# Performance work log

Measured on AMD Instinct MI355X. Metric: run time of the kernel, lower is better.

The kernel has to match this reference:

```python
import jax, jax.numpy as jnp
import numpy as np

N_NODES = 20000
N_EDGES = 320000
N_GRAPHS = 64
NEG_SLOPE = 0.2
BN_EPS = 1e-5


def setup_inputs() -> dict:
    key = jax.random.key(0)
    ks = jax.random.split(key, 32)
    inp = {}
    inp['x'] = jax.random.normal(ks[0], (N_NODES, 9), jnp.float32)
    inp['global_feat'] = jax.random.normal(ks[1], (N_GRAPHS, 20), jnp.float32)
    inp['edge_index'] = jax.random.randint(ks[2], (2, N_EDGES), 0, N_NODES, jnp.int32)
    inp['batch'] = jnp.sort(jax.random.randint(ks[3], (N_NODES,), 0, N_GRAPHS, jnp.int32))
    s = 0.1  # modest init scale for numerical sanity
    inp['W_l1'] = jax.random.normal(ks[4], (9, 256), jnp.float32) * s
    inp['b_l1'] = jax.random.normal(ks[5], (256,), jnp.float32) * s
    inp['W_r1'] = jax.random.normal(ks[6], (9, 256), jnp.float32) * s
    inp['b_r1'] = jax.random.normal(ks[7], (256,), jnp.float32) * s
    inp['att1'] = jax.random.normal(ks[8], (4, 64), jnp.float32) * s
    inp['bias1'] = jax.random.normal(ks[9], (256,), jnp.float32) * s
    inp['bn1_gamma'] = jnp.ones((256,), jnp.float32)
    inp['bn1_beta'] = jnp.zeros((256,), jnp.float32)
    inp['bn1_mean'] = jax.random.normal(ks[10], (256,), jnp.float32) * s
    inp['bn1_var'] = jax.random.uniform(ks[11], (256,), jnp.float32, 0.5, 1.5)
    inp['W_l2'] = jax.random.normal(ks[12], (256, 512), jnp.float32) * s
    inp['b_l2'] = jax.random.normal(ks[13], (512,), jnp.float32) * s
    inp['W_r2'] = jax.random.normal(ks[14], (256, 512), jnp.float32) * s
    inp['b_r2'] = jax.random.normal(ks[15], (512,), jnp.float32) * s
    inp['att2'] = jax.random.normal(ks[16], (4, 128), jnp.float32) * s
    inp['bias2'] = jax.random.normal(ks[17], (512,), jnp.float32) * s
    inp['bn2_gamma'] = jnp.ones((512,), jnp.float32)
    inp['bn2_beta'] = jnp.zeros((512,), jnp.float32)
    inp['bn2_mean'] = jax.random.normal(ks[18], (512,), jnp.float32) * s
    inp['bn2_var'] = jax.random.uniform(ks[19], (512,), jnp.float32, 0.5, 1.5)
    inp['fc1_W'] = jax.random.normal(ks[20], (532, 128), jnp.float32) * s
    inp['fc1_b'] = jax.random.normal(ks[21], (128,), jnp.float32) * s
    inp['fc2_W'] = jax.random.normal(ks[22], (128, 1), jnp.float32) * s
    inp['fc2_b'] = jax.random.normal(ks[23], (1,), jnp.float32) * s
    return inp


def _gatv2(x, src, dst, W_l, b_l, W_r, b_r, att, bias, H, C):
    N = x.shape[0]
    xl = (x @ W_l + b_l).reshape(N, H, C)  # source transform
    xr = (x @ W_r + b_r).reshape(N, H, C)  # target transform
    m = xl[src] + xr[dst]                               # [E,H,C]
    e = jnp.sum(jax.nn.leaky_relu(m, NEG_SLOPE) * att, axis=-1)  # [E,H]
    emax = jax.ops.segment_max(e, dst, num_segments=N)
    ex = jnp.exp(e - emax[dst])
    denom = jax.ops.segment_sum(ex, dst, num_segments=N)
    alpha = ex / denom[dst]                             # segment softmax over incoming edges
    out = jax.ops.segment_sum(alpha[..., None] * xl[src], dst, num_segments=N)
    return out.reshape(N, H * C) + bias


def _bn_eval(x, gamma, beta, mean, var):
    return (x - mean) * jax.lax.rsqrt(var + BN_EPS) * gamma + beta


def reference(x, global_feat, edge_index, batch,
              W_l1, b_l1, W_r1, b_r1, att1, bias1,
              bn1_gamma, bn1_beta, bn1_mean, bn1_var,
              W_l2, b_l2, W_r2, b_r2, att2, bias2,
              bn2_gamma, bn2_beta, bn2_mean, bn2_var,
              fc1_W, fc1_b, fc2_W, fc2_b):
    N = x.shape[0]
    # PyG GATv2Conv default: add self loops
    loop = jnp.arange(N, dtype=edge_index.dtype)
    src = jnp.concatenate([edge_index[0], loop])
    dst = jnp.concatenate([edge_index[1], loop])
    h = _gatv2(x, src, dst, W_l1, b_l1, W_r1, b_r1, att1, bias1, 4, 64)
    h = jax.nn.relu(_bn_eval(h, bn1_gamma, bn1_beta, bn1_mean, bn1_var))
    h = _gatv2(h, src, dst, W_l2, b_l2, W_r2, b_r2, att2, bias2, 4, 128)
    h = jax.nn.relu(_bn_eval(h, bn2_gamma, bn2_beta, bn2_mean, bn2_var))
    # global mean pool over graphs
    B = global_feat.shape[0]
    sums = jax.ops.segment_sum(h, batch, num_segments=B)
    cnts = jax.ops.segment_sum(jnp.ones((N, 1), h.dtype), batch, num_segments=B)
    pooled = sums / jnp.maximum(cnts, 1.0)
    z = jnp.concatenate([pooled, global_feat], axis=1)  # [B, 532]
    z = jax.nn.relu(z @ fc1_W + fc1_b)  # dropout is identity at inference
    return (z @ fc2_W + fc2_b).squeeze(-1)  # [B]
```

## Files before the change

### kernel.cpp

```cpp
#include <hip/hip_runtime.h>


typedef _Float16 half2v __attribute__((ext_vector_type(2)));
typedef _Float16 half8v __attribute__((ext_vector_type(8)));
typedef __attribute__((ext_vector_type(4))) float floatx4;

#define SLOT_STRIDE 96

template <int CPL> struct VecSel;
template <> struct VecSel<4> { using T = uint2; };
template <> struct VecSel<8> { using T = uint4; };

__device__ inline unsigned short f2h(float v) {
    return __builtin_bit_cast(unsigned short, (_Float16)v);
}
__device__ inline half2v u2h2(unsigned u) { return __builtin_bit_cast(half2v, u); }
__device__ inline unsigned h22u(half2v h) { return __builtin_bit_cast(unsigned, h); }
__device__ inline unsigned packh2(float a, float b) {
    half2v h; h[0] = (_Float16)a; h[1] = (_Float16)b;
    return h22u(h);
}

__device__ inline float fdot2f(half2v a, half2v b, float c) {
#if __has_builtin(__builtin_amdgcn_fdot2)
    return __builtin_amdgcn_fdot2(a, b, c, false);
#else
    return c + (float)a[0] * (float)b[0] + (float)a[1] * (float)b[1];
#endif
}


#define L1_NODES 32

__global__ void k_setup(const int* __restrict__ ei, int E0, int N, int B,
                        int* __restrict__ counts, int* __restrict__ slots,
                        const int* __restrict__ batch, int* __restrict__ goff,
                        const float* __restrict__ x,
                        const float* __restrict__ Wl1, const float* __restrict__ bl1,
                        const float* __restrict__ Wr1, const float* __restrict__ br1,
                        unsigned short* __restrict__ xl1, unsigned short* __restrict__ xr1,
                        const float* __restrict__ Wl2, const float* __restrict__ Wr2,
                        unsigned short* __restrict__ Wlt, unsigned short* __restrict__ Wrt) {
    __shared__ char smem[8320];
    int E = E0 + N;
    int SC = (E + 255) >> 8;
    int L1B = (N + L1_NODES - 1) / L1_NODES;
    int bid = blockIdx.x;
    int t = threadIdx.x;

    if (bid < SC) {
        int e = bid * 256 + t;
        if (e >= E) return;
        int s, d;
        if (e < E0) { s = ei[e]; d = ei[E0 + e]; } else { s = e - E0; d = s; }
        int pos = atomicAdd(&counts[d], 1);
        if (pos < SLOT_STRIDE) slots[d * SLOT_STRIDE + pos] = s;
    } else if (bid < SC + L1B) {
        float (*xs)[9] = reinterpret_cast<float(*)[9]>(smem);
        int nb = (bid - SC) * L1_NODES;
        int h = t >> 7, p = t & 127;
        for (int i = t; i < L1_NODES * 9; i += 256) {
            int node = nb + i / 9;
            xs[i / 9][i % 9] = (node < N) ? x[node * 9 + i % 9] : 0.f;
        }
        __syncthreads();
        int c0 = 2 * p, c1 = 2 * p + 1;
        float wl0[9], wl1[9], wr0[9], wr1[9];
#pragma unroll
        for (int k = 0; k < 9; k++) {
            wl0[k] = Wl1[k * 256 + c0]; wl1[k] = Wl1[k * 256 + c1];
            wr0[k] = Wr1[k * 256 + c0]; wr1[k] = Wr1[k * 256 + c1];
        }
        float b0 = bl1[c0], b1 = bl1[c1], r0b = br1[c0], r1b = br1[c1];
        for (int j = h * 16; j < h * 16 + 16; j++) {
            int node = nb + j;
            if (node >= N) break;
            float a0 = b0, a1 = b1, r0 = r0b, r1 = r1b;
#pragma unroll
            for (int k = 0; k < 9; k++) {
                float xv = xs[j][k];
                a0 += xv * wl0[k]; a1 += xv * wl1[k];
                r0 += xv * wr0[k]; r1 += xv * wr1[k];
            }
            *reinterpret_cast<unsigned*>(xl1 + (size_t)node * 256 + c0) = packh2(a0, a1);
            *reinterpret_cast<unsigned*>(xr1 + (size_t)node * 256 + c0) = packh2(r0, r1);
        }
    } else if (bid < SC + L1B + 64) {
        unsigned short (*tile)[65] = reinterpret_cast<unsigned short(*)[65]>(smem);
        int idx = bid - SC - L1B;
        int tx = idx & 7, ty = (idx >> 3) & 3, tz = idx >> 5;
        const float* W = tz ? Wr2 : Wl2;
        unsigned short* Wt = tz ? Wrt : Wlt;
        int k0 = ty * 64, n0 = tx * 64;
        int tn = t & 63, tq = t >> 6;
#pragma unroll
        for (int i = 0; i < 16; i++) {
            int k = tq * 16 + i;
            tile[k][tn] = f2h(W[(size_t)(k0 + k) * 512 + n0 + tn]);
        }
        __syncthreads();
#pragma unroll
        for (int i = 0; i < 16; i++) {
            int nn = tq * 16 + i;
            Wt[(size_t)(n0 + nn) * 256 + k0 + tn] = tile[tn][nn];
        }
    } else {
        int n = (bid - SC - L1B - 64) * 256 + t;
        if (n >= N) return;
        int b = batch[n];
        int prev = (n == 0) ? -1 : batch[n - 1];
        for (int g = prev + 1; g <= b; g++) goff[g] = n;
        if (n == N - 1)
            for (int g = b + 1; g <= B; g++) goff[g] = N;
    }
}


template <int CPL>
__global__ void k_gat_agg(const unsigned short* __restrict__ xl,
                          const unsigned short* __restrict__ xr,
                          const float* __restrict__ att, const float* __restrict__ bias,
                          const float* __restrict__ gamma, const float* __restrict__ beta,
                          const float* __restrict__ mean, const float* __restrict__ var,
                          const int* __restrict__ counts, const int* __restrict__ slots,
                          unsigned short* __restrict__ hout, int N) {
    const int HC = 64 * CPL;
    const int V = CPL / 2;
    using VecT = typename VecSel<CPL>::T;
    int wave = (blockIdx.x * blockDim.x + threadIdx.x) >> 6;
    int lane = threadIdx.x & 63;
    if (wave >= N) return;
    int n = wave;
    int cbase = lane * CPL;

    half2v xr2[V], at2[V], acc[V];
    {
        unsigned r[V];
        if constexpr (CPL == 8) {
            uint4 q = *reinterpret_cast<const uint4*>(xr + (size_t)n * HC + cbase);
            r[0] = q.x; r[1] = q.y; r[2] = q.z; r[3] = q.w;
        } else {
            uint2 q = *reinterpret_cast<const uint2*>(xr + (size_t)n * HC + cbase);
            r[0] = q.x; r[1] = q.y;
        }
#pragma unroll
        for (int v = 0; v < V; v++) {
            xr2[v] = u2h2(r[v]);
            at2[v][0] = (_Float16)att[cbase + 2 * v];
            at2[v][1] = (_Float16)att[cbase + 2 * v + 1];
            acc[v] = (half2v){(_Float16)0.f, (_Float16)0.f};
        }
    }
    const half2v c02 = {(_Float16)0.2f, (_Float16)0.2f};

    int deg = counts[n];
    deg = deg < SLOT_STRIDE ? deg : SLOT_STRIDE;
    const int* sl = slots + (size_t)n * SLOT_STRIDE;
    const unsigned short* xlb = xl + cbase;
    float m = -1e30f, l = 0.f;

    VecT qA = *reinterpret_cast<const VecT*>(xlb + (size_t)sl[0] * HC);
    VecT qB = (deg > 1) ? *reinterpret_cast<const VecT*>(xlb + (size_t)sl[1] * HC) : qA;

    int slot = 0;
    while (slot + 1 < deg) {
        VecT ra = qA, rb = qB;
        int p2 = slot + 2 < deg ? slot + 2 : deg - 1;
        int p3 = slot + 3 < deg ? slot + 3 : deg - 1;
        qA = *reinterpret_cast<const VecT*>(xlb + (size_t)sl[p2] * HC);
        qB = *reinterpret_cast<const VecT*>(xlb + (size_t)sl[p3] * HC);

        half2v ah[V], bh[V];
        {
            unsigned ua[V], ub[V];
            if constexpr (CPL == 8) {
                ua[0] = ra.x; ua[1] = ra.y; ua[2] = ra.z; ua[3] = ra.w;
                ub[0] = rb.x; ub[1] = rb.y; ub[2] = rb.z; ub[3] = rb.w;
            } else {
                ua[0] = ra.x; ua[1] = ra.y;
                ub[0] = rb.x; ub[1] = rb.y;
            }
#pragma unroll
            for (int v = 0; v < V; v++) { ah[v] = u2h2(ua[v]); bh[v] = u2h2(ub[v]); }
        }
        float pa = 0.f, pb = 0.f;
#pragma unroll
        for (int v = 0; v < V; v++) {
            half2v ta = ah[v] + xr2[v];
            half2v la = __builtin_elementwise_max(ta, ta * c02);
            pa = fdot2f(la, at2[v], pa);
            half2v tb = bh[v] + xr2[v];
            half2v lb = __builtin_elementwise_max(tb, tb * c02);
            pb = fdot2f(lb, at2[v], pb);
        }
        pa += __shfl_xor(pa, 1);  pb += __shfl_xor(pb, 1);
        pa += __shfl_xor(pa, 2);  pb += __shfl_xor(pb, 2);
        pa += __shfl_xor(pa, 4);  pb += __shfl_xor(pb, 4);
        pa += __shfl_xor(pa, 8);  pb += __shfl_xor(pb, 8);
        float pm = fmaxf(pa, pb);
        if (__all(pm <= m + 4.f)) {
            float wa = __expf(pa - m), wb = __expf(pb - m);
            l += wa + wb;
            _Float16 wah = (_Float16)wa, wbh = (_Float16)wb;
            half2v wa2 = {wah, wah}, wb2 = {wbh, wbh};
#pragma unroll
            for (int v = 0; v < V; v++) {
                acc[v] = ah[v] * wa2 + acc[v];
                acc[v] = bh[v] * wb2 + acc[v];
            }
        } else {
            float mn = fmaxf(m, pm);
            float sc = __expf(m - mn);
            float wa = __expf(pa - mn), wb = __expf(pb - mn);
            l = l * sc + wa + wb;
            _Float16 sch = (_Float16)sc, wah = (_Float16)wa, wbh = (_Float16)wb;
            half2v sc2 = {sch, sch}, wa2 = {wah, wah}, wb2 = {wbh, wbh};
#pragma unroll
            for (int v = 0; v < V; v++) {
                acc[v] = ah[v] * wa2 + acc[v] * sc2;
                acc[v] = bh[v] * wb2 + acc[v];
            }
            m = mn;
        }
        slot += 2;
    }
    if (slot < deg) {
        half2v ah[V];
        {
            unsigned ua[V];
            if constexpr (CPL == 8) {
                ua[0] = qA.x; ua[1] = qA.y; ua[2] = qA.z; ua[3] = qA.w;
            } else {
                ua[0] = qA.x; ua[1] = qA.y;
            }
#pragma unroll
            for (int v = 0; v < V; v++) ah[v] = u2h2(ua[v]);
        }
        float pa = 0.f;
#pragma unroll
        for (int v = 0; v < V; v++) {
            half2v ta = ah[v] + xr2[v];
            half2v la = __builtin_elementwise_max(ta, ta * c02);
            pa = fdot2f(la, at2[v], pa);
        }
        pa += __shfl_xor(pa, 1);
        pa += __shfl_xor(pa, 2);
        pa += __shfl_xor(pa, 4);
        pa += __shfl_xor(pa, 8);
        if (__all(pa <= m + 4.f)) {
            float wa = __expf(pa - m);
            l += wa;
            _Float16 wah = (_Float16)wa;
            half2v wa2 = {wah, wah};
#pragma unroll
            for (int v = 0; v < V; v++) acc[v] = ah[v] * wa2 + acc[v];
        } else {
            float mn = fmaxf(m, pa);
            float sc = __expf(m - mn);
            float wa = __expf(pa - mn);
            l = l * sc + wa;
            _Float16 sch = (_Float16)sc, wah = (_Float16)wa;
            half2v sc2 = {sch, sch}, wa2 = {wah, wah};
#pragma unroll
            for (int v = 0; v < V; v++) acc[v] = ah[v] * wa2 + acc[v] * sc2;
            m = mn;
        }
    }

    float inv = 1.f / l;
    unsigned ow[V];
#pragma unroll
    for (int v = 0; v < V; v++) {
        half2v o;
#pragma unroll
        for (int j = 0; j < 2; j++) {
            int c = cbase + 2 * v + j;
            float val = (float)acc[v][j] * inv + bias[c];
            val = (val - mean[c]) * rsqrtf(var[c] + 1e-5f) * gamma[c] + beta[c];
            o[j] = (_Float16)fmaxf(val, 0.f);
        }
        ow[v] = h22u(o);
    }
    unsigned short* dst = hout + (size_t)n * HC + cbase;
    if constexpr (CPL == 8)
        *reinterpret_cast<uint4*>(dst) = *reinterpret_cast<uint4*>(ow);
    else
        *reinterpret_cast<uint2*>(dst) = *reinterpret_cast<uint2*>(ow);
}


__global__ __launch_bounds__(256) void k_gemm_mfma(
    const unsigned short* __restrict__ A,
    const unsigned short* __restrict__ Wlt,
    const unsigned short* __restrict__ Wrt,
    const float* __restrict__ bl, const float* __restrict__ br,
    unsigned short* __restrict__ Cl, unsigned short* __restrict__ Cr,
    int M) {
    const int K = 256, NCOL = 512;
    __shared__ unsigned short lds[2][2][128 * 32];
    int side = blockIdx.z;
    const unsigned short* Bmat = side ? Wrt : Wlt;
    const float* bias = side ? br : bl;
    unsigned short* C = side ? Cr : Cl;
    int bm = blockIdx.y * 128, bn = blockIdx.x * 128;
    int t = threadIdx.x;
    int lane = t & 63;
    int wid = t >> 6;
    int wr = wid >> 1, wc = wid & 1;

    floatx4 acc[4][4];
#pragma unroll
    for (int m = 0; m < 4; m++)
#pragma unroll
        for (int n = 0; n < 4; n++) acc[m][n] = (floatx4){0.f, 0.f, 0.f, 0.f};

    auto stage = [&](int buf, int k0) {
#pragma unroll
        for (int i = 0; i < 2; i++) {
            int c = i * 256 + t;
            int row = c >> 2;
            int kk = ((c & 3) << 3) ^ (((row >> 1) & 3) << 3);
            int gm = bm + row; gm = gm < M ? gm : M - 1;
            const unsigned short* gA = A + (size_t)gm * K + k0 + kk;
            __builtin_amdgcn_global_load_lds(
                (const __attribute__((address_space(1))) void*)gA,
                (__attribute__((address_space(3))) void*)&lds[buf][0][c * 8], 16, 0, 0);
            int gn = bn + row;
            const unsigned short* gB = Bmat + (size_t)gn * K + k0 + kk;
            __builtin_amdgcn_global_load_lds(
                (const __attribute__((address_space(1))) void*)gB,
                (__attribute__((address_space(3))) void*)&lds[buf][1][c * 8], 16, 0, 0);
        }
    };

    stage(0, 0);
    __syncthreads();
    int q = lane >> 4, rl = lane & 15;
    for (int ks = 0; ks < 8; ks++) {
        int buf = ks & 1;
        if (ks < 7) stage(buf ^ 1, (ks + 1) * 32);
        half8v a[4], b[4];
#pragma unroll
        for (int m = 0; m < 4; m++) {
            int row = wr * 64 + m * 16 + rl;
            int colb = (q * 16) ^ (((row >> 1) & 3) << 4);
            a[m] = *reinterpret_cast<const half8v*>(
                reinterpret_cast<const char*>(&lds[buf][0][0]) + row * 64 + colb);
        }
#pragma unroll
        for (int n = 0; n < 4; n++) {
            int row = wc * 64 + n * 16 + rl;
            int colb = (q * 16) ^ (((row >> 1) & 3) << 4);
            b[n] = *reinterpret_cast<const half8v*>(
                reinterpret_cast<const char*>(&lds[buf][1][0]) + row * 64 + colb);
        }
#pragma unroll
        for (int m = 0; m < 4; m++)
#pragma unroll
            for (int n = 0; n < 4; n++)
                acc[m][n] = __builtin_amdgcn_mfma_f32_16x16x32_f16(a[m], b[n], acc[m][n], 0, 0, 0);
        __syncthreads();
    }
#pragma unroll
    for (int m = 0; m < 4; m++) {
#pragma unroll
        for (int n = 0; n < 4; n++) {
            int gn = bn + wc * 64 + n * 16 + rl;
            float bv = bias[gn];
#pragma unroll
            for (int r = 0; r < 4; r++) {
                int gm = bm + wr * 64 + m * 16 + q * 4 + r;
                if (gm < M) C[(size_t)gm * NCOL + gn] = f2h(acc[m][n][r] + bv);
            }
        }
    }
}


#define POOL_CHUNKS 32

__global__ void k_pool_partial(const unsigned short* __restrict__ h2,
                               const int* __restrict__ goff,
                               float* __restrict__ partial) {
    int g = blockIdx.x, c = blockIdx.y;
    int t = threadIdx.x;
    int n0 = goff[g], n1 = goff[g + 1];
    int len = n1 - n0;
    int c0 = n0 + (int)(((long long)len * c) / POOL_CHUNKS);
    int c1 = n0 + (int)(((long long)len * (c + 1)) / POOL_CHUNKS);
    float s0 = 0.f, s1 = 0.f;
    for (int n = c0; n < c1; n++) {
        half2v h = u2h2(*reinterpret_cast<const unsigned*>(h2 + (size_t)n * 512 + t * 2));
        s0 += (float)h[0]; s1 += (float)h[1];
    }
    float* p = partial + ((size_t)g * POOL_CHUNKS + c) * 512;
    p[t * 2] = s0;
    p[t * 2 + 1] = s1;
}


__global__ void k_pool_head(const float* __restrict__ partial,
                            const int* __restrict__ goff,
                            const float* __restrict__ gf,
                            const float* __restrict__ W1, const float* __restrict__ b1,
                            const float* __restrict__ W2, const float* __restrict__ b2,
                            float* __restrict__ out) {
    int g = blockIdx.x;
    int t = threadIdx.x;
    __shared__ float z[532];
    __shared__ float red[128];
    float s = 0.f;
#pragma unroll
    for (int c = 0; c < POOL_CHUNKS; c++)
        s += partial[((size_t)g * POOL_CHUNKS + c) * 512 + t];
    float inv = 1.f / fmaxf((float)(goff[g + 1] - goff[g]), 1.f);
    z[t] = s * inv;
    if (t < 20) z[512 + t] = gf[g * 20 + t];
    __syncthreads();
    if (t < 128) {
        float a = b1[t];
        for (int k = 0; k < 532; k++) a += z[k] * W1[k * 128 + t];
        red[t] = fmaxf(a, 0.f) * W2[t];
    }
    __syncthreads();
    if (t < 64) {
        float v = red[t] + red[t + 64];
#pragma unroll
        for (int sdown = 32; sdown; sdown >>= 1) v += __shfl_down(v, sdown);
        if (t == 0) out[g] = v + b2[0];
    }
}


extern "C" void kernel_launch(void* const* d_in, const int* in_sizes, int n_in,
                              void* d_out, int out_size, void* d_ws, size_t ws_size,
                              hipStream_t stream) {
    const float* x       = (const float*)d_in[0];
    const float* gfeat   = (const float*)d_in[1];
    const int*   ei      = (const int*)d_in[2];
    const int*   batch   = (const int*)d_in[3];
    const float* W_l1    = (const float*)d_in[4];
    const float* b_l1    = (const float*)d_in[5];
    const float* W_r1    = (const float*)d_in[6];
    const float* b_r1    = (const float*)d_in[7];
    const float* att1    = (const float*)d_in[8];
    const float* bias1   = (const float*)d_in[9];
    const float* bn1_g   = (const float*)d_in[10];
    const float* bn1_b   = (const float*)d_in[11];
    const float* bn1_m   = (const float*)d_in[12];
    const float* bn1_v   = (const float*)d_in[13];
    const float* W_l2    = (const float*)d_in[14];
    const float* b_l2    = (const float*)d_in[15];
    const float* W_r2    = (const float*)d_in[16];
    const float* b_r2    = (const float*)d_in[17];
    const float* att2    = (const float*)d_in[18];
    const float* bias2   = (const float*)d_in[19];
    const float* bn2_g   = (const float*)d_in[20];
    const float* bn2_b   = (const float*)d_in[21];
    const float* bn2_m   = (const float*)d_in[22];
    const float* bn2_v   = (const float*)d_in[23];
    const float* fc1_W   = (const float*)d_in[24];
    const float* fc1_b   = (const float*)d_in[25];
    const float* fc2_W   = (const float*)d_in[26];
    const float* fc2_b   = (const float*)d_in[27];
    float* out = (float*)d_out;

    const int N  = in_sizes[0] / 9;
    const int B  = in_sizes[1] / 20;
    const int E0 = in_sizes[2] / 2;
    const int E  = E0 + N;

    char* ws = (char*)d_ws;
    const size_t SZ256 = (size_t)N * 256 * 2;
    const size_t SZ512 = (size_t)N * 512 * 2;
    unsigned short* xl1 = (unsigned short*)(ws);
    unsigned short* xr1 = (unsigned short*)(ws + SZ256);
    unsigned short* h1  = (unsigned short*)(ws + 2 * SZ256);
    unsigned short* xl2 = (unsigned short*)(ws + 3 * SZ256);
    unsigned short* xr2 = (unsigned short*)(ws + 3 * SZ256 + SZ512);
    unsigned short* h2  = (unsigned short*)(ws + 3 * SZ256 + 2 * SZ512);
    size_t o = 3 * SZ256 + 3 * SZ512;
    unsigned short* Wlt = (unsigned short*)(ws + o);
    unsigned short* Wrt = (unsigned short*)(ws + o + 262144);
    size_t oi = o + 2 * 262144;
    int* counts = (int*)(ws + oi);
    int* goff   = (int*)(ws + oi + 80000);
    int* slots  = (int*)(ws + oi + 80000 + 384);
    size_t op = oi + 80000 + 384 + (size_t)N * SLOT_STRIDE * 4;
    float* partial = (float*)(ws + op);
    (void)ws_size; (void)n_in; (void)out_size;

    (void)hipMemsetAsync(ws + oi, 0, 80000, stream);

    int SC = (E + 255) / 256;
    int L1B = (N + L1_NODES - 1) / L1_NODES;
    int GB = (N + 255) / 256;
    k_setup<<<SC + L1B + 64 + GB, 256, 0, stream>>>(
        ei, E0, N, B, counts, slots, batch, goff,
        x, W_l1, b_l1, W_r1, b_r1, xl1, xr1, W_l2, W_r2, Wlt, Wrt);

    k_gat_agg<4><<<(N * 64 + 255) / 256, 256, 0, stream>>>(
        xl1, xr1, att1, bias1, bn1_g, bn1_b, bn1_m, bn1_v, counts, slots, h1, N);

    dim3 ggrid(512 / 128, (N + 127) / 128, 2);
    k_gemm_mfma<<<ggrid, 256, 0, stream>>>(h1, Wlt, Wrt, b_l2, b_r2, xl2, xr2, N);

    k_gat_agg<8><<<(N * 64 + 255) / 256, 256, 0, stream>>>(
        xl2, xr2, att2, bias2, bn2_g, bn2_b, bn2_m, bn2_v, counts, slots, h2, N);

    k_pool_partial<<<dim3(B, POOL_CHUNKS), 256, 0, stream>>>(h2, goff, partial);
    k_pool_head<<<B, 512, 0, stream>>>(partial, goff, gfeat,
                                       fc1_W, fc1_b, fc2_W, fc2_b, out);
}
```

Baseline: 170.2 us.

## Sort nodes by degree and use persistent grid-stride waves in GAT aggregation

Adds a single-block counting-sort kernel that orders nodes by in-degree. Both aggregation kernels become persistent, with a fixed grid of 2048 blocks whose waves loop over nodes in that degree order. The aim is to balance work, since waves in a block then handle similar degrees and tail imbalance shrinks. The cost is an extra serial single-block launch, plus less locality for the xr reads and hout writes.

Result: slower. 193.6 us (+13.7%).

```diff
diff --git a/kernel.cpp b/kernel.cpp
--- a/kernel.cpp
+++ b/kernel.cpp
@@ -6,6 +6,7 @@
 typedef __attribute__((ext_vector_type(4))) float floatx4;
 
 #define SLOT_STRIDE 96
+#define AGG_BLOCKS 2048
 
 template <int CPL> struct VecSel;
 template <> struct VecSel<4> { using T = uint2; };
@@ -116,176 +117,206 @@
 }
 
 
+__global__ void k_degsort(const int* __restrict__ counts, int* __restrict__ order, int N) {
+    __shared__ int bins[128];
+    __shared__ int base[128];
+    int t = threadIdx.x;
+    if (t < 128) bins[t] = 0;
+    __syncthreads();
+    for (int n = t; n < N; n += 1024) {
+        int d = counts[n]; d = d > 96 ? 96 : d;
+        atomicAdd(&bins[d], 1);
+    }
+    __syncthreads();
+    if (t == 0) {
+        int s = 0;
+        for (int i = 0; i < 128; i++) { base[i] = s; s += bins[i]; }
+    }
+    __syncthreads();
+    if (t < 128) bins[t] = 0;
+    __syncthreads();
+    for (int n = t; n < N; n += 1024) {
+        int d = counts[n]; d = d > 96 ? 96 : d;
+        int p = atomicAdd(&bins[d], 1);
+        order[base[d] + p] = n;
+    }
+}
+
+
 template <int CPL>
-__global__ void k_gat_agg(const unsigned short* __restrict__ xl,
-                          const unsigned short* __restrict__ xr,
-                          const float* __restrict__ att, const float* __restrict__ bias,
-                          const float* __restrict__ gamma, const float* __restrict__ beta,
-                          const float* __restrict__ mean, const float* __restrict__ var,
-                          const int* __restrict__ counts, const int* __restrict__ slots,
-                          unsigned short* __restrict__ hout, int N) {
+__global__ __launch_bounds__(256) void k_gat_agg(
+        const unsigned short* __restrict__ xl,
+        const unsigned short* __restrict__ xr,
+        const float* __restrict__ att, const float* __restrict__ bias,
+        const float* __restrict__ gamma, const float* __restrict__ beta,
+        const float* __restrict__ mean, const float* __restrict__ var,
+        const int* __restrict__ counts, const int* __restrict__ slots,
+        const int* __restrict__ order,
+        unsigned short* __restrict__ hout, int N) {
     const int HC = 64 * CPL;
     const int V = CPL / 2;
     using VecT = typename VecSel<CPL>::T;
-    int wave = (blockIdx.x * blockDim.x + threadIdx.x) >> 6;
+    int gw = (blockIdx.x * blockDim.x + threadIdx.x) >> 6;
     int lane = threadIdx.x & 63;
-    if (wave >= N) return;
-    int n = wave;
+    const int GW = AGG_BLOCKS * 4;
     int cbase = lane * CPL;
 
-    half2v xr2[V], at2[V], acc[V];
-    {
-        unsigned r[V];
-        if constexpr (CPL == 8) {
-            uint4 q = *reinterpret_cast<const uint4*>(xr + (size_t)n * HC + cbase);
-            r[0] = q.x; r[1] = q.y; r[2] = q.z; r[3] = q.w;
-        } else {
-            uint2 q = *reinterpret_cast<const uint2*>(xr + (size_t)n * HC + cbase);
-            r[0] = q.x; r[1] = q.y;
-        }
+    half2v at2[V];
+#pragma unroll
+    for (int v = 0; v < V; v++) {
+        at2[v][0] = (_Float16)att[cbase + 2 * v];
+        at2[v][1] = (_Float16)att[cbase + 2 * v + 1];
+    }
+    const half2v c02 = {(_Float16)0.2f, (_Float16)0.2f};
+
+    for (int i = gw; i < N; i += GW) {
+        int n = order[i];
+        half2v xr2[V], acc[V];
+        {
+            VecT q = *reinterpret_cast<const VecT*>(xr + (size_t)n * HC + cbase);
+            unsigned r[V];
+            if constexpr (CPL == 8) { r[0] = q.x; r[1] = q.y; r[2] = q.z; r[3] = q.w; }
+            else { r[0] = q.x; r[1] = q.y; }
+#pragma unroll
+            for (int v = 0; v < V; v++) {
+                xr2[v] = u2h2(r[v]);
+                acc[v] = (half2v){(_Float16)0.f, (_Float16)0.f};
+            }
+        }
+        int deg = counts[n];
+        deg = deg < SLOT_STRIDE ? deg : SLOT_STRIDE;
+        const int* sl = slots + (size_t)n * SLOT_STRIDE;
+        const unsigned short* xlb = xl + cbase;
+        float m = -1e30f, l = 0.f;
+
+        VecT qA = *reinterpret_cast<const VecT*>(xlb + (size_t)sl[0] * HC);
+        VecT qB = (deg > 1) ? *reinterpret_cast<const VecT*>(xlb + (size_t)sl[1] * HC) : qA;
+
+        int slot = 0;
+        while (slot + 1 < deg) {
+            VecT ra = qA, rb = qB;
+            int p2 = slot + 2 < deg ? slot + 2 : deg - 1;
+            int p3 = slot + 3 < deg ? slot + 3 : deg - 1;
+            qA = *reinterpret_cast<const VecT*>(xlb + (size_t)sl[p2] * HC);
+            qB = *reinterpret_cast<const VecT*>(xlb + (size_t)sl[p3] * HC);
+
+            half2v ah[V], bh[V];
+            {
+                unsigned ua[V], ub[V];
+                if constexpr (CPL == 8) {
+                    ua[0] = ra.x; ua[1] = ra.y; ua[2] = ra.z; ua[3] = ra.w;
+                    ub[0] = rb.x; ub[1] = rb.y; ub[2] = rb.z; ub[3] = rb.w;
+                } else {
+                    ua[0] = ra.x; ua[1] = ra.y;
+                    ub[0] = rb.x; ub[1] = rb.y;
+                }
+#pragma unroll
+                for (int v = 0; v < V; v++) { ah[v] = u2h2(ua[v]); bh[v] = u2h2(ub[v]); }
+            }
+            float pa = 0.f, pb = 0.f;
+#pragma unroll
+            for (int v = 0; v < V; v++) {
+                half2v ta = ah[v] + xr2[v];
+                half2v la = __builtin_elementwise_max(ta, ta * c02);
+                pa = fdot2f(la, at2[v], pa);
+                half2v tb = bh[v] + xr2[v];
+                half2v lb = __builtin_elementwise_max(tb, tb * c02);
+                pb = fdot2f(lb, at2[v], pb);
+            }
+            pa += __shfl_xor(pa, 1);  pb += __shfl_xor(pb, 1);
+            pa += __shfl_xor(pa, 2);  pb += __shfl_xor(pb, 2);
+            pa += __shfl_xor(pa, 4);  pb += __shfl_xor(pb, 4);
+            pa += __shfl_xor(pa, 8);  pb += __shfl_xor(pb, 8);
+            float pm = fmaxf(pa, pb);
+            if (__all(pm <= m + 4.f)) {
+                float wa = __expf(pa - m), wb = __expf(pb - m);
+                l += wa + wb;
+                _Float16 wah = (_Float16)wa, wbh = (_Float16)wb;
+                half2v wa2 = {wah, wah}, wb2 = {wbh, wbh};
+#pragma unroll
+                for (int v = 0; v < V; v++) {
+                    acc[v] = ah[v] * wa2 + acc[v];
+                    acc[v] = bh[v] * wb2 + acc[v];
+                }
+            } else {
+                float mn = fmaxf(m, pm);
+                float sc = __expf(m - mn);
+                float wa = __expf(pa - mn), wb = __expf(pb - mn);
+                l = l * sc + wa + wb;
+                _Float16 sch = (_Float16)sc, wah = (_Float16)wa, wbh = (_Float16)wb;
+                half2v sc2 = {sch, sch}, wa2 = {wah, wah}, wb2 = {wbh, wbh};
+#pragma unroll
+                for (int v = 0; v < V; v++) {
+                    acc[v] = ah[v] * wa2 + acc[v] * sc2;
+                    acc[v] = bh[v] * wb2 + acc[v];
+                }
+                m = mn;
+            }
+            slot += 2;
+        }
+        if (slot < deg) {
+            half2v ah[V];
+            {
+                unsigned ua[V];
+                if constexpr (CPL == 8) {
+                    ua[0] = qA.x; ua[1] = qA.y; ua[2] = qA.z; ua[3] = qA.w;
+                } else {
+                    ua[0] = qA.x; ua[1] = qA.y;
+                }
+#pragma unroll
+                for (int v = 0; v < V; v++) ah[v] = u2h2(ua[v]);
+            }
+            float pa = 0.f;
+#pragma unroll
+            for (int v = 0; v < V; v++) {
+                half2v ta = ah[v] + xr2[v];
+                half2v la = __builtin_elementwise_max(ta, ta * c02);
+                pa = fdot2f(la, at2[v], pa);
+            }
+            pa += __shfl_xor(pa, 1);
+            pa += __shfl_xor(pa, 2);
+            pa += __shfl_xor(pa, 4);
+            pa += __shfl_xor(pa, 8);
+            if (__all(pa <= m + 4.f)) {
+                float wa = __expf(pa - m);
+                l += wa;
+                _Float16 wah = (_Float16)wa;
+                half2v wa2 = {wah, wah};
+#pragma unroll
+                for (int v = 0; v < V; v++) acc[v] = ah[v] * wa2 + acc[v];
+            } else {
+                float mn = fmaxf(m, pa);
+                float sc = __expf(m - mn);
+                float wa = __expf(pa - mn);
+                l = l * sc + wa;
+                _Float16 sch = (_Float16)sc, wah = (_Float16)wa;
+                half2v sc2 = {sch, sch}, wa2 = {wah, wah};
+#pragma unroll
+                for (int v = 0; v < V; v++) acc[v] = ah[v] * wa2 + acc[v] * sc2;
+                m = mn;
+            }
+        }
+
+        float inv = 1.f / l;
+        unsigned ow[V];
 #pragma unroll
         for (int v = 0; v < V; v++) {
-            xr2[v] = u2h2(r[v]);
-            at2[v][0] = (_Float16)att[cbase + 2 * v];
-            at2[v][1] = (_Float16)att[cbase + 2 * v + 1];
-            acc[v] = (half2v){(_Float16)0.f, (_Float16)0.f};
-        }
-    }
-    const half2v c02 = {(_Float16)0.2f, (_Float16)0.2f};
-
-    int deg = counts[n];
-    deg = deg < SLOT_STRIDE ? deg : SLOT_STRIDE;
-    const int* sl = slots + (size_t)n * SLOT_STRIDE;
-    const unsigned short* xlb = xl + cbase;
-    float m = -1e30f, l = 0.f;
-
-    VecT qA = *reinterpret_cast<const VecT*>(xlb + (size_t)sl[0] * HC);
-    VecT qB = (deg > 1) ? *reinterpret_cast<const VecT*>(xlb + (size_t)sl[1] * HC) : qA;
-
-    int slot = 0;
-    while (slot + 1 < deg) {
-        VecT ra = qA, rb = qB;
-        int p2 = slot + 2 < deg ? slot + 2 : deg - 1;
-        int p3 = slot + 3 < deg ? slot + 3 : deg - 1;
-        qA = *reinterpret_cast<const VecT*>(xlb + (size_t)sl[p2] * HC);
-        qB = *reinterpret_cast<const VecT*>(xlb + (size_t)sl[p3] * HC);
-
-        half2v ah[V], bh[V];
-        {
-            unsigned ua[V], ub[V];
-            if constexpr (CPL == 8) {
-                ua[0] = ra.x; ua[1] = ra.y; ua[2] = ra.z; ua[3] = ra.w;
-                ub[0] = rb.x; ub[1] = rb.y; ub[2] = rb.z; ub[3] = rb.w;
-            } else {
-                ua[0] = ra.x; ua[1] = ra.y;
-                ub[0] = rb.x; ub[1] = rb.y;
-            }
-#pragma unroll
-            for (int v = 0; v < V; v++) { ah[v] = u2h2(ua[v]); bh[v] = u2h2(ub[v]); }
-        }
-        float pa = 0.f, pb = 0.f;
-#pragma unroll
-        for (int v = 0; v < V; v++) {
-            half2v ta = ah[v] + xr2[v];
-            half2v la = __builtin_elementwise_max(ta, ta * c02);
-            pa = fdot2f(la, at2[v], pa);
-            half2v tb = bh[v] + xr2[v];
-            half2v lb = __builtin_elementwise_max(tb, tb * c02);
-            pb = fdot2f(lb, at2[v], pb);
-        }
-        pa += __shfl_xor(pa, 1);  pb += __shfl_xor(pb, 1);
-        pa += __shfl_xor(pa, 2);  pb += __shfl_xor(pb, 2);
-        pa += __shfl_xor(pa, 4);  pb += __shfl_xor(pb, 4);
-        pa += __shfl_xor(pa, 8);  pb += __shfl_xor(pb, 8);
-        float pm = fmaxf(pa, pb);
-        if (__all(pm <= m + 4.f)) {
-            float wa = __expf(pa - m), wb = __expf(pb - m);
-            l += wa + wb;
-            _Float16 wah = (_Float16)wa, wbh = (_Float16)wb;
-            half2v wa2 = {wah, wah}, wb2 = {wbh, wbh};
-#pragma unroll
-            for (int v = 0; v < V; v++) {
-                acc[v] = ah[v] * wa2 + acc[v];
-                acc[v] = bh[v] * wb2 + acc[v];
-            }
-        } else {
-            float mn = fmaxf(m, pm);
-            float sc = __expf(m - mn);
-            float wa = __expf(pa - mn), wb = __expf(pb - mn);
-            l = l * sc + wa + wb;
-            _Float16 sch = (_Float16)sc, wah = (_Float16)wa, wbh = (_Float16)wb;
-            half2v sc2 = {sch, sch}, wa2 = {wah, wah}, wb2 = {wbh, wbh};
-#pragma unroll
-            for (int v = 0; v < V; v++) {
-                acc[v] = ah[v] * wa2 + acc[v] * sc2;
-                acc[v] = bh[v] * wb2 + acc[v];
-            }
-            m = mn;
-        }
-        slot += 2;
-    }
-    if (slot < deg) {
-        half2v ah[V];
-        {
-            unsigned ua[V];
-            if constexpr (CPL == 8) {
-                ua[0] = qA.x; ua[1] = qA.y; ua[2] = qA.z; ua[3] = qA.w;
-            } else {
-                ua[0] = qA.x; ua[1] = qA.y;
-            }
-#pragma unroll
-            for (int v = 0; v < V; v++) ah[v] = u2h2(ua[v]);
-        }
-        float pa = 0.f;
-#pragma unroll
-        for (int v = 0; v < V; v++) {
-            half2v ta = ah[v] + xr2[v];
-            half2v la = __builtin_elementwise_max(ta, ta * c02);
-            pa = fdot2f(la, at2[v], pa);
-        }
-        pa += __shfl_xor(pa, 1);
-        pa += __shfl_xor(pa, 2);
-        pa += __shfl_xor(pa, 4);
-        pa += __shfl_xor(pa, 8);
-        if (__all(pa <= m + 4.f)) {
-            float wa = __expf(pa - m);
-            l += wa;
-            _Float16 wah = (_Float16)wa;
-            half2v wa2 = {wah, wah};
-#pragma unroll
-            for (int v = 0; v < V; v++) acc[v] = ah[v] * wa2 + acc[v];
-        } else {
-            float mn = fmaxf(m, pa);
-            float sc = __expf(m - mn);
-            float wa = __expf(pa - mn);
-            l = l * sc + wa;
-            _Float16 sch = (_Float16)sc, wah = (_Float16)wa;
-            half2v sc2 = {sch, sch}, wa2 = {wah, wah};
-#pragma unroll
-            for (int v = 0; v < V; v++) acc[v] = ah[v] * wa2 + acc[v] * sc2;
-            m = mn;
-        }
-    }
-
-    float inv = 1.f / l;
-    unsigned ow[V];
-#pragma unroll
-    for (int v = 0; v < V; v++) {
-        half2v o;
-#pragma unroll
-        for (int j = 0; j < 2; j++) {
-            int c = cbase + 2 * v + j;
-            float val = (float)acc[v][j] * inv + bias[c];
-            val = (val - mean[c]) * rsqrtf(var[c] + 1e-5f) * gamma[c] + beta[c];
-            o[j] = (_Float16)fmaxf(val, 0.f);
-        }
-        ow[v] = h22u(o);
-    }
-    unsigned short* dst = hout + (size_t)n * HC + cbase;
-    if constexpr (CPL == 8)
-        *reinterpret_cast<uint4*>(dst) = *reinterpret_cast<uint4*>(ow);
-    else
-        *reinterpret_cast<uint2*>(dst) = *reinterpret_cast<uint2*>(ow);
+            half2v o;
+#pragma unroll
+            for (int j = 0; j < 2; j++) {
+                int c = cbase + 2 * v + j;
+                float val = (float)acc[v][j] * inv + bias[c];
+                val = (val - mean[c]) * rsqrtf(var[c] + 1e-5f) * gamma[c] + beta[c];
+                o[j] = (_Float16)fmaxf(val, 0.f);
+            }
+            ow[v] = h22u(o);
+        }
+        unsigned short* dst = hout + (size_t)n * HC + cbase;
+        if constexpr (CPL == 8)
+            *reinterpret_cast<uint4*>(dst) = *reinterpret_cast<uint4*>(ow);
+        else
+            *reinterpret_cast<uint2*>(dst) = *reinterpret_cast<uint2*>(ow);
+    }
 }
 
 
@@ -485,8 +516,9 @@
     size_t oi = o + 2 * 262144;
     int* counts = (int*)(ws + oi);
     int* goff   = (int*)(ws + oi + 80000);
-    int* slots  = (int*)(ws + oi + 80000 + 384);
-    size_t op = oi + 80000 + 384 + (size_t)N * SLOT_STRIDE * 4;
+    int* order  = (int*)(ws + oi + 80000 + 384);
+    int* slots  = (int*)(ws + oi + 80000 + 384 + 80000);
+    size_t op = oi + 80000 + 384 + 80000 + (size_t)N * SLOT_STRIDE * 4;
     float* partial = (float*)(ws + op);
     (void)ws_size; (void)n_in; (void)out_size;
 
@@ -499,14 +531,16 @@
         ei, E0, N, B, counts, slots, batch, goff,
         x, W_l1, b_l1, W_r1, b_r1, xl1, xr1, W_l2, W_r2, Wlt, Wrt);
 
-    k_gat_agg<4><<<(N * 64 + 255) / 256, 256, 0, stream>>>(
-        xl1, xr1, att1, bias1, bn1_g, bn1_b, bn1_m, bn1_v, counts, slots, h1, N);
+    k_degsort<<<1, 1024, 0, stream>>>(counts, order, N);
+
+    k_gat_agg<4><<<AGG_BLOCKS, 256, 0, stream>>>(
+        xl1, xr1, att1, bias1, bn1_g, bn1_b, bn1_m, bn1_v, counts, slots, order, h1, N);
 
     dim3 ggrid(512 / 128, (N + 127) / 128, 2);
     k_gemm_mfma<<<ggrid, 256, 0, stream>>>(h1, Wlt, Wrt, b_l2, b_r2, xl2, xr2, N);
 
-    k_gat_agg<8><<<(N * 64 + 255) / 256, 256, 0, stream>>>(
-        xl2, xr2, att2, bias2, bn2_g, bn2_b, bn2_m, bn2_v, counts, slots, h2, N);
+    k_gat_agg<8><<<AGG_BLOCKS, 256, 0, stream>>>(
+        xl2, xr2, att2, bias2, bn2_g, bn2_b, bn2_m, bn2_v, counts, slots, order, h2, N);
 
     k_pool_partial<<<dim3(B, POOL_CHUNKS), 256, 0, stream>>>(h2, goff, partial);
     k_pool_head<<<B, 512, 0, stream>>>(partial, goff, gfeat,
```
